# Kernel tuning notes

Hardware: AMD Instinct MI355X
Metric: run time of the kernel (lower is better)

## Reference

```python
import jax, jax.numpy as jnp
import numpy as np
from jax import lax

# Geometry constants (stand-in for beijing* globals)
A = 96           # beijingAngleNum
P = 4            # beijingPlanes
DET0, DET1 = 256, 8   # beijingSubDetectorSize [u, v]
NZ, NY, NX = 32, 256, 256  # beijingVolumeSize (nz = P * DET1)
T = 256          # ray integration steps
LAMB = 0.01


def _bilinear(vol, ix, iy):
    # vol: [nz, ny, nx]; ix, iy: [...] index-space coords. Zero outside.
    nz, ny, nx = vol.shape
    x0 = jnp.floor(ix); y0 = jnp.floor(iy)
    fx = (ix - x0).astype(vol.dtype); fy = (iy - y0).astype(vol.dtype)
    x0i = x0.astype(jnp.int32); y0i = y0.astype(jnp.int32)

    def g(yi, xi):
        valid = ((xi >= 0) & (xi < nx) & (yi >= 0) & (yi < ny)).astype(vol.dtype)
        v = vol[:, jnp.clip(yi, 0, ny - 1), jnp.clip(xi, 0, nx - 1)]  # [nz, ...]
        return v * valid

    return (g(y0i, x0i) * (1 - fy) * (1 - fx)
            + g(y0i, x0i + 1) * (1 - fy) * fx
            + g(y0i + 1, x0i) * fy * (1 - fx)
            + g(y0i + 1, x0i + 1) * fy * fx)


def forward_project(vol):
    # vol: [NZ, NY, NX] -> sinogram [A, NZ, DET0], parallel-beam over 180 deg
    angles = jnp.arange(A, dtype=jnp.float32) * (np.pi / A)
    u = jnp.arange(DET0, dtype=jnp.float32) - (DET0 - 1) / 2.0  # detector coord
    t = jnp.arange(T, dtype=jnp.float32) - (T - 1) / 2.0        # along-ray coord

    def per_angle(_, th):
        c, s = jnp.cos(th), jnp.sin(th)
        x = -u[:, None] * s + t[None, :] * c   # [DET0, T]
        y = u[:, None] * c + t[None, :] * s
        samp = _bilinear(vol, x + (NX - 1) / 2.0, y + (NY - 1) / 2.0)  # [NZ,DET0,T]
        return None, samp.sum(-1)  # line integral, [NZ, DET0]

    _, S = lax.scan(per_angle, None, angles)
    return S  # [A, NZ, DET0]


def back_project(S):
    # S: [A, NZ, DET0] -> volume [NZ, NY, NX] (adjoint-style backprojection)
    angles = jnp.arange(A, dtype=jnp.float32) * (np.pi / A)
    yy = jnp.arange(NY, dtype=jnp.float32) - (NY - 1) / 2.0
    xx = jnp.arange(NX, dtype=jnp.float32) - (NX - 1) / 2.0
    Y, X = jnp.meshgrid(yy, xx, indexing='ij')  # [NY, NX]

    def per_angle(acc, inp):
        th, Sa = inp  # Sa: [NZ, DET0]
        c, s = jnp.cos(th), jnp.sin(th)
        ub = -X * s + Y * c + (DET0 - 1) / 2.0  # detector bin coord [NY,NX]
        u0 = jnp.floor(ub)
        fu = (ub - u0).astype(Sa.dtype)
        u0i = u0.astype(jnp.int32)

        def g(ui):
            valid = ((ui >= 0) & (ui < DET0)).astype(Sa.dtype)
            return Sa[:, jnp.clip(ui, 0, DET0 - 1)] * valid  # [NZ,NY,NX]

        val = g(u0i) * (1 - fu) + g(u0i + 1) * fu
        return acc + val, None

    vol0 = jnp.zeros((NZ, NY, NX), dtype=S.dtype)
    vol, _ = lax.scan(per_angle, vol0, (angles, S))
    return vol


def setup_inputs() -> dict:
    key = jax.random.key(0)
    k1, k2 = jax.random.split(key)
    x = jax.random.normal(k1, (1, 1, NZ, NY, NX), dtype=jnp.float32)
    p = jax.random.normal(k2, (1, 1, A * P, DET1, DET0), dtype=jnp.float32)
    return {"x": x, "p": p}


def reference(x, p):
    vol = x[0, 0]                              # [NZ, NY, NX]
    S = forward_project(vol)                   # [A, NZ, DET0] native
    # ForwardProjection wrapper: (A,P,V,U) -> permute -> flat external layout
    ext = S.reshape(A, P, DET1, DET0).transpose(0, 2, 1, 3).reshape(1, 1, A * P, DET1, DET0)
    residual = ext - p
    # BackProjection wrapper: undo external layout back to native
    res_native = residual.reshape(A, DET1, P, DET0).transpose(0, 2, 1, 3).reshape(A, NZ, DET0)
    volb = back_project(res_native)            # [NZ, NY, NX]
    return (-LAMB * volb)[None, None]          # [1,1,NZ,NY,NX]
```

## Files before the change

### kernel.cpp

```cpp
#include <hip/hip_runtime.h>
#include <hip/hip_fp16.h>

#define A     96
#define DET0  256
#define NZ    32
#define NY    256
#define NX    256
#define T     256
#define LAMB  0.01f

#define TRIG_OFF  0
#define REST_OFF  256
#define VOLB_OFF  786688
#define PART_OFF  1835264
#define RES_ELEMS 786432

__device__ __forceinline__ void accp(float* acc, unsigned v, float w) {
    __half2 h = *reinterpret_cast<__half2*>(&v);
    acc[0] = fmaf(w, __low2float(h),  acc[0]);
    acc[1] = fmaf(w, __high2float(h), acc[1]);
}
__device__ __forceinline__ void acc8h(float* acc, uint4 q, float w) {
    accp(acc + 0, q.x, w);
    accp(acc + 2, q.y, w);
    accp(acc + 4, q.z, w);
    accp(acc + 6, q.w, w);
}

__global__ __launch_bounds__(256) void k_transpose(const float* __restrict__ src,
                                                   unsigned short* __restrict__ vol_h,
                                                   float* __restrict__ trig,
                                                   const float* __restrict__ p,
                                                   float* __restrict__ res_t) {
    __shared__ float lds[64 * 33];
    const int y   = blockIdx.y;
    const int x0  = blockIdx.x * 64;
    const int tid = threadIdx.x;

    if (blockIdx.x == 0 && y == 0 && tid < A) {
        float th = (float)tid * (float)(3.14159265358979323846 / (double)A);
        trig[2 * tid]     = cosf(th);
        trig[2 * tid + 1] = sinf(th);
    }

    const int xr = tid & 63;
    const int zr = tid >> 6;
    #pragma unroll
    for (int pz = 0; pz < 8; ++pz) {
        int z = pz * 4 + zr;
        lds[xr * 33 + z] = src[(z * NY + y) * NX + x0 + xr];
    }
    __syncthreads();
    const int zw = tid & 31;
    const int xw = tid >> 5;
    #pragma unroll
    for (int px = 0; px < 8; ++px) {
        int xi = px * 8 + xw;
        vol_h[(y * NX + x0 + xi) * NZ + zw] =
            __half_as_ushort(__float2half(lds[xi * 33 + zw]));
    }

    if (y < A) {
        const int a  = y;
        const int u0 = blockIdx.x * 64;
        __syncthreads();
        const int col = tid & 63;
        const int r0  = tid >> 6;
        #pragma unroll
        for (int i = 0; i < 8; ++i) {
            int r = i * 4 + r0;
            lds[r * 65 + col] = p[a * 8192 + r * 256 + u0 + col];
        }
        __syncthreads();
        const int ul = tid >> 2;
        const int zb = (tid & 3) * 8;
        float o[8];
        #pragma unroll
        for (int k = 0; k < 8; ++k) {
            int z = zb + k;
            int r = ((z & 7) << 2) + (z >> 3);
            o[k] = -lds[r * 65 + ul];
        }
        float4* d = (float4*)(res_t + (a * DET0 + u0 + ul) * NZ + zb);
        d[0] = make_float4(o[0], o[1], o[2], o[3]);
        d[1] = make_float4(o[4], o[5], o[6], o[7]);
    }
}

__device__ __forceinline__ void rng(float g, float b, float L, float H,
                                    float& lo, float& hi) {
    if (fabsf(g) > 1e-5f) {
        float r0 = (L - b) / g, r1 = (H - b) / g;
        lo = fminf(r0, r1); hi = fmaxf(r0, r1);
    } else {
        bool in = (b >= L && b <= H);
        lo = in ? -1e9f : 1e9f;
        hi = in ? 1e9f : -1e9f;
    }
}
__device__ __forceinline__ int clampi(float v) {
    return (int)fminf(fmaxf(v, -2.f), 258.f);
}

__device__ __forceinline__ void sample_edge(const char* base, float ix, float iy,
                                            float* acc) {
    float xf = floorf(ix), yf = floorf(iy);
    float fx = ix - xf, fy = iy - yf;
    int x0 = (int)xf, y0 = (int)yf;
    float wx0 = 1.f - fx, wx1 = fx, wy0 = 1.f - fy, wy1 = fy;
    if ((unsigned)x0 >= NX)       wx0 = 0.f;
    if ((unsigned)(x0 + 1) >= NX) wx1 = 0.f;
    if ((unsigned)y0 >= NY)       wy0 = 0.f;
    if ((unsigned)(y0 + 1) >= NY) wy1 = 0.f;
    if ((wx0 == 0.f && wx1 == 0.f) || (wy0 == 0.f && wy1 == 0.f)) return;
    int cx0 = min(max(x0, 0), NX - 1);
    int cx1 = min(max(x0 + 1, 0), NX - 1);
    int cy0 = min(max(y0, 0), NY - 1);
    int cy1 = min(max(y0 + 1, 0), NY - 1);
    uint4 q00 = *(const uint4*)(base + ((size_t)((cy0 << 8) + cx0) << 6));
    uint4 q01 = *(const uint4*)(base + ((size_t)((cy0 << 8) + cx1) << 6));
    uint4 q10 = *(const uint4*)(base + ((size_t)((cy1 << 8) + cx0) << 6));
    uint4 q11 = *(const uint4*)(base + ((size_t)((cy1 << 8) + cx1) << 6));
    acc8h(acc, q00, wy0 * wx0);
    acc8h(acc, q01, wy0 * wx1);
    acc8h(acc, q10, wy1 * wx0);
    acc8h(acc, q11, wy1 * wx1);
}

__global__ __launch_bounds__(256) void k_forward(const unsigned short* __restrict__ vol_h,
                                                 const float* __restrict__ trig,
                                                 float* __restrict__ part) {
    const int tid = threadIdx.x;
    const int a   = blockIdx.z;
    const int u   = blockIdx.x * 64 + (tid >> 2);
    const int zq  = tid & 3;
    const int cid = blockIdx.y;
    const int C   = gridDim.y;

    const float c = trig[2 * a];
    const float s = trig[2 * a + 1];
    const float uu = (float)u - 127.5f;
    const float bx = fmaf(-uu, s, 127.5f);
    const float by = fmaf(uu, c, 127.5f);

    float lo1, hi1, lo2, hi2;
    rng(c, bx, -1.f, 256.f, lo1, hi1);
    rng(s, by, -1.f, 256.f, lo2, hi2);
    float fl = fmaxf(lo1, lo2), fh = fminf(hi1, hi2);
    int F0 = max(0,     clampi(ceilf(fl + 127.5f)));
    int F1 = min(T - 1, clampi(floorf(fh + 127.5f)));
    int len = F1 - F0 + 1; if (len < 0) len = 0;
    int b0 = F0 + (len * cid) / C;
    int b1 = F0 + (len * (cid + 1)) / C - 1;
    rng(c, bx, 1.f, 253.5f, lo1, hi1);
    rng(s, by, 1.f, 253.5f, lo2, hi2);
    float il = fmaxf(lo1, lo2), ih = fminf(hi1, hi2);
    int tI0 = max(clampi(ceilf(il + 127.5f)) + 1, b0);
    int tI1 = min(clampi(floorf(ih + 127.5f)) - 1, b1);
    if (tI0 > tI1) { tI0 = b1 + 1; tI1 = b1; }

    const char* base = (const char*)vol_h + zq * 16;
    float acc[8];
    #pragma unroll
    for (int k = 0; k < 8; ++k) acc[k] = 0.f;

    for (int t = b0; t < tI0; ++t) {
        float ttf = (float)t - 127.5f;
        sample_edge(base, fmaf(ttf, c, bx), fmaf(ttf, s, by), acc);
    }

    if (tI0 <= tI1) {
        float ttf = (float)tI0 - 127.5f;
        float ix = fmaf(ttf, c, bx);
        float iy = fmaf(ttf, s, by);
        float xf = floorf(ix), yf = floorf(iy);
        float fxc = ix - xf, fyc = iy - yf;
        const char* p0 = base + ((size_t)(((int)yf << 8) + (int)xf) << 6);
        uint4 c00 = *(const uint4*)(p0);
        uint4 c01 = *(const uint4*)(p0 + 64);
        uint4 c10 = *(const uint4*)(p0 + 16384);
        uint4 c11 = *(const uint4*)(p0 + 16384 + 64);
        for (int t = tI0; t <= tI1; ++t) {
            float ttn = (float)(t + 1) - 127.5f;
            float ixn = fmaf(ttn, c, bx);
            float iyn = fmaf(ttn, s, by);
            float xfn = floorf(ixn), yfn = floorf(iyn);
            float fxn = ixn - xfn, fyn = iyn - yfn;
            const char* pn = base + ((size_t)(((int)yfn << 8) + (int)xfn) << 6);
            uint4 n00 = *(const uint4*)(pn);
            uint4 n01 = *(const uint4*)(pn + 64);
            uint4 n10 = *(const uint4*)(pn + 16384);
            uint4 n11 = *(const uint4*)(pn + 16384 + 64);
            float wx0 = 1.f - fxc, wy0 = 1.f - fyc;
            acc8h(acc, c00, wy0 * wx0);
            acc8h(acc, c01, wy0 * fxc);
            acc8h(acc, c10, fyc * wx0);
            acc8h(acc, c11, fyc * fxc);
            c00 = n00; c01 = n01; c10 = n10; c11 = n11;
            fxc = fxn; fyc = fyn;
        }
    }

    for (int t = tI1 + 1; t <= b1; ++t) {
        float ttf = (float)t - 127.5f;
        sample_edge(base, fmaf(ttf, c, bx), fmaf(ttf, s, by), acc);
    }

    float4* dst = (float4*)(part + (size_t)cid * RES_ELEMS +
                            ((a * DET0 + u) * NZ + zq * 8));
    dst[0] = make_float4(acc[0], acc[1], acc[2], acc[3]);
    dst[1] = make_float4(acc[4], acc[5], acc[6], acc[7]);
}

__global__ __launch_bounds__(256) void k_combine(const float* __restrict__ part,
                                                 float* __restrict__ res_t,
                                                 int C) {
    const int j4 = blockIdx.x * 256 + threadIdx.x;
    float4 v = ((const float4*)res_t)[j4];
    for (int c = 0; c < C; ++c) {
        float4 w = ((const float4*)(part + (size_t)c * RES_ELEMS))[j4];
        v.x += w.x; v.y += w.y; v.z += w.z; v.w += w.w;
    }
    ((float4*)res_t)[j4] = v;
}

__global__ __launch_bounds__(256) void k_backward(const float* __restrict__ res_t,
                                                  const float* __restrict__ trig,
                                                  float* __restrict__ out) {
    __shared__ float2 wbw[A * 32];
    __shared__ int    wbo[A * 32];
    __shared__ float  ob[32 * 33];
    const int tid = threadIdx.x;
    const int y  = blockIdx.y;
    const int xb = blockIdx.x * 32;

    for (int e = tid; e < A * 32; e += 256) {
        int a  = e >> 5;
        int xs = e & 31;
        float cc = trig[2 * a];
        float ss = trig[2 * a + 1];
        float xx = (float)(xb + xs) - 127.5f;
        float yy = (float)y - 127.5f;
        float ub = fmaf(-xx, ss, fmaf(yy, cc, 127.5f));
        float uf = floorf(ub);
        float fu = ub - uf;
        int i0 = (int)uf;
        float w0 = ((unsigned)i0 < DET0) ? (1.f - fu) : 0.f;
        float w1 = ((unsigned)(i0 + 1) < DET0) ? fu : 0.f;
        int c1 = min(max(i0 + 1, 0), DET0);
        wbw[e] = make_float2(w0, w1);
        wbo[e] = ((a * DET0 + c1) * NZ - NZ) << 2;
    }
    __syncthreads();

    const int xs = tid >> 3;
    const int zq = tid & 7;
    const char* rbase = (const char*)res_t + zq * 16;
    float4 acc = make_float4(0.f, 0.f, 0.f, 0.f);
    #pragma unroll 4
    for (int a = 0; a < A; ++a) {
        float2 w  = wbw[a * 32 + xs];
        int   off = wbo[a * 32 + xs];
        float4 v0 = *(const float4*)(rbase + off);
        float4 v1 = *(const float4*)(rbase + off + 128);
        acc.x = fmaf(w.x, v0.x, fmaf(w.y, v1.x, acc.x));
        acc.y = fmaf(w.x, v0.y, fmaf(w.y, v1.y, acc.y));
        acc.z = fmaf(w.x, v0.z, fmaf(w.y, v1.z, acc.z));
        acc.w = fmaf(w.x, v0.w, fmaf(w.y, v1.w, acc.w));
    }

    ob[(zq * 4 + 0) * 33 + xs] = acc.x;
    ob[(zq * 4 + 1) * 33 + xs] = acc.y;
    ob[(zq * 4 + 2) * 33 + xs] = acc.z;
    ob[(zq * 4 + 3) * 33 + xs] = acc.w;
    __syncthreads();

    const int z  = tid >> 3;
    const int x4 = (tid & 7) * 4;
    float4 o = make_float4(ob[z * 33 + x4],     ob[z * 33 + x4 + 1],
                           ob[z * 33 + x4 + 2], ob[z * 33 + x4 + 3]);
    float4* dst = (float4*)(out + (size_t)z * (NY * NX) + y * NX + xb + x4);
    *dst = make_float4(-LAMB * o.x, -LAMB * o.y, -LAMB * o.z, -LAMB * o.w);
}

extern "C" void kernel_launch(void* const* d_in, const int* in_sizes, int n_in,
                              void* d_out, int out_size, void* d_ws, size_t ws_size,
                              hipStream_t stream) {
    const float* x = (const float*)d_in[0];
    const float* p = (const float*)d_in[1];
    float* out = (float*)d_out;
    float* ws  = (float*)d_ws;

    float*          trig  = ws + TRIG_OFF;
    float*          res_t = ws + REST_OFF;
    unsigned short* vol_h = (unsigned short*)(ws + VOLB_OFF);
    float*          part  = ws + PART_OFF;

    size_t avail = ws_size / 4;
    int C = 8;
    while (C > 1 && (size_t)PART_OFF + (size_t)C * RES_ELEMS > avail) C >>= 1;

    k_transpose<<<dim3(NX / 64, NY), 256, 0, stream>>>(x, vol_h, trig, p, res_t);
    k_forward  <<<dim3(4, C, A), 256, 0, stream>>>(vol_h, trig, part);
    k_combine  <<<dim3(RES_ELEMS / 4 / 256), 256, 0, stream>>>(part, res_t, C);
    k_backward <<<dim3(NX / 32, NY), 256, 0, stream>>>(res_t, trig, out);
}
```

Baseline: 192.8 us.

## Compute backprojection weights inline over 4 rows per block; pin forward loop schedule

The backward kernel no longer precomputes per-angle weights and offsets into shared memory. Each thread now computes them inline and handles four output rows, so one block covers a 32x4 tile and the grid shrinks fourfold. This removes the shared-memory setup phase and its barrier and adds more independent loads per thread. It costs more registers and repeats the trig math per row. In the forward kernel the interior loop is kept rolled and a scheduling barrier is placed between the next-sample loads and the current-sample FMAs to hold the software-pipelined order.

```diff
diff --git a/kernel.cpp b/kernel.cpp
--- a/kernel.cpp
+++ b/kernel.cpp
@@ -180,6 +180,7 @@
         uint4 c01 = *(const uint4*)(p0 + 64);
         uint4 c10 = *(const uint4*)(p0 + 16384);
         uint4 c11 = *(const uint4*)(p0 + 16384 + 64);
+        #pragma unroll 1
         for (int t = tI0; t <= tI1; ++t) {
             float ttn = (float)(t + 1) - 127.5f;
             float ixn = fmaf(ttn, c, bx);
@@ -191,6 +192,7 @@
             uint4 n01 = *(const uint4*)(pn + 64);
             uint4 n10 = *(const uint4*)(pn + 16384);
             uint4 n11 = *(const uint4*)(pn + 16384 + 64);
+            __builtin_amdgcn_sched_barrier(0);
             float wx0 = 1.f - fxc, wy0 = 1.f - fyc;
             acc8h(acc, c00, wy0 * wx0);
             acc8h(acc, c01, wy0 * fxc);
@@ -227,60 +229,57 @@
 __global__ __launch_bounds__(256) void k_backward(const float* __restrict__ res_t,
                                                   const float* __restrict__ trig,
                                                   float* __restrict__ out) {
-    __shared__ float2 wbw[A * 32];
-    __shared__ int    wbo[A * 32];
-    __shared__ float  ob[32 * 33];
+    __shared__ float ob[32 * 33];
     const int tid = threadIdx.x;
-    const int y  = blockIdx.y;
+    const int y0 = blockIdx.y * 4;
     const int xb = blockIdx.x * 32;
-
-    for (int e = tid; e < A * 32; e += 256) {
-        int a  = e >> 5;
-        int xs = e & 31;
-        float cc = trig[2 * a];
-        float ss = trig[2 * a + 1];
-        float xx = (float)(xb + xs) - 127.5f;
-        float yy = (float)y - 127.5f;
-        float ub = fmaf(-xx, ss, fmaf(yy, cc, 127.5f));
-        float uf = floorf(ub);
-        float fu = ub - uf;
-        int i0 = (int)uf;
-        float w0 = ((unsigned)i0 < DET0) ? (1.f - fu) : 0.f;
-        float w1 = ((unsigned)(i0 + 1) < DET0) ? fu : 0.f;
-        int c1 = min(max(i0 + 1, 0), DET0);
-        wbw[e] = make_float2(w0, w1);
-        wbo[e] = ((a * DET0 + c1) * NZ - NZ) << 2;
-    }
-    __syncthreads();
-
     const int xs = tid >> 3;
     const int zq = tid & 7;
     const char* rbase = (const char*)res_t + zq * 16;
-    float4 acc = make_float4(0.f, 0.f, 0.f, 0.f);
-    #pragma unroll 4
+    const float xx = (float)(xb + xs) - 127.5f;
+
+    float4 acc[4];
+    #pragma unroll
+    for (int yt = 0; yt < 4; ++yt) acc[yt] = make_float4(0.f, 0.f, 0.f, 0.f);
+
     for (int a = 0; a < A; ++a) {
-        float2 w  = wbw[a * 32 + xs];
-        int   off = wbo[a * 32 + xs];
-        float4 v0 = *(const float4*)(rbase + off);
-        float4 v1 = *(const float4*)(rbase + off + 128);
-        acc.x = fmaf(w.x, v0.x, fmaf(w.y, v1.x, acc.x));
-        acc.y = fmaf(w.x, v0.y, fmaf(w.y, v1.y, acc.y));
-        acc.z = fmaf(w.x, v0.z, fmaf(w.y, v1.z, acc.z));
-        acc.w = fmaf(w.x, v0.w, fmaf(w.y, v1.w, acc.w));
-    }
-
-    ob[(zq * 4 + 0) * 33 + xs] = acc.x;
-    ob[(zq * 4 + 1) * 33 + xs] = acc.y;
-    ob[(zq * 4 + 2) * 33 + xs] = acc.z;
-    ob[(zq * 4 + 3) * 33 + xs] = acc.w;
-    __syncthreads();
-
-    const int z  = tid >> 3;
-    const int x4 = (tid & 7) * 4;
-    float4 o = make_float4(ob[z * 33 + x4],     ob[z * 33 + x4 + 1],
-                           ob[z * 33 + x4 + 2], ob[z * 33 + x4 + 3]);
-    float4* dst = (float4*)(out + (size_t)z * (NY * NX) + y * NX + xb + x4);
-    *dst = make_float4(-LAMB * o.x, -LAMB * o.y, -LAMB * o.z, -LAMB * o.w);
+        float cc = trig[2 * a];
+        float ss = trig[2 * a + 1];
+        #pragma unroll
+        for (int yt = 0; yt < 4; ++yt) {
+            float yy = (float)(y0 + yt) - 127.5f;
+            float ub = fmaf(-xx, ss, fmaf(yy, cc, 127.5f));
+            float uf = floorf(ub);
+            float fu = ub - uf;
+            int i0 = (int)uf;
+            float w0 = ((unsigned)i0 < DET0) ? (1.f - fu) : 0.f;
+            float w1 = ((unsigned)(i0 + 1) < DET0) ? fu : 0.f;
+            int c1 = min(max(i0 + 1, 0), DET0);
+            int off = ((a * DET0 + c1) * NZ - NZ) << 2;
+            float4 v0 = *(const float4*)(rbase + off);
+            float4 v1 = *(const float4*)(rbase + off + 128);
+            acc[yt].x = fmaf(w0, v0.x, fmaf(w1, v1.x, acc[yt].x));
+            acc[yt].y = fmaf(w0, v0.y, fmaf(w1, v1.y, acc[yt].y));
+            acc[yt].z = fmaf(w0, v0.z, fmaf(w1, v1.z, acc[yt].z));
+            acc[yt].w = fmaf(w0, v0.w, fmaf(w1, v1.w, acc[yt].w));
+        }
+    }
+
+    #pragma unroll 1
+    for (int yt = 0; yt < 4; ++yt) {
+        __syncthreads();
+        ob[(zq * 4 + 0) * 33 + xs] = acc[yt].x;
+        ob[(zq * 4 + 1) * 33 + xs] = acc[yt].y;
+        ob[(zq * 4 + 2) * 33 + xs] = acc[yt].z;
+        ob[(zq * 4 + 3) * 33 + xs] = acc[yt].w;
+        __syncthreads();
+        int z  = tid >> 3;
+        int x4 = (tid & 7) * 4;
+        float4 o = make_float4(ob[z * 33 + x4],     ob[z * 33 + x4 + 1],
+                               ob[z * 33 + x4 + 2], ob[z * 33 + x4 + 3]);
+        float4* dst = (float4*)(out + (size_t)z * (NY * NX) + (y0 + yt) * NX + xb + x4);
+        *dst = make_float4(-LAMB * o.x, -LAMB * o.y, -LAMB * o.z, -LAMB * o.w);
+    }
 }
 
 extern "C" void kernel_launch(void* const* d_in, const int* in_sizes, int n_in,
@@ -303,5 +302,5 @@
     k_transpose<<<dim3(NX / 64, NY), 256, 0, stream>>>(x, vol_h, trig, p, res_t);
     k_forward  <<<dim3(4, C, A), 256, 0, stream>>>(vol_h, trig, part);
     k_combine  <<<dim3(RES_ELEMS / 4 / 256), 256, 0, stream>>>(part, res_t, C);
-    k_backward <<<dim3(NX / 32, NY), 256, 0, stream>>>(res_t, trig, out);
-}
+    k_backward <<<dim3(NX / 32, NY / 4), 256, 0, stream>>>(res_t, trig, out);
+}
```

Result: slower. 230.9 us (+19.8%).
